# Kernel optimization log

Measured on AMD Instinct MI355X. Metric: run time of the kernel, lower is better.

Reference implementation:

```python
import jax, jax.numpy as jnp
import numpy as np

N = 100000      # nodes
E = 1600000     # edges (avg degree 16)
D_IN = 256
H = 128         # hidden_dim
D_OUT = 64
BN_EPS = 1e-5


def setup_inputs() -> dict:
    key = jax.random.key(0)
    ks = jax.random.split(key, 16)
    s = 0.05  # small init scale
    x = jax.random.normal(ks[0], (N, D_IN), jnp.float32)
    edge_index = jax.random.randint(ks[1], (2, E), 0, N)
    inp = {
        "x": x,
        "edge_index": edge_index,
        "w_in": jax.random.normal(ks[2], (D_IN, H), jnp.float32) * s,
        "b_in": jnp.zeros((H,), jnp.float32),
        # SAGEConv layer 1: lin_l (neighbors, with bias) + lin_r (self, no bias)
        "w_l1": jax.random.normal(ks[3], (H, H), jnp.float32) * s,
        "b_l1": jnp.zeros((H,), jnp.float32),
        "w_r1": jax.random.normal(ks[4], (H, H), jnp.float32) * s,
        "g1": jnp.ones((H,), jnp.float32),
        "be1": jnp.zeros((H,), jnp.float32),
        # SAGEConv layer 2
        "w_l2": jax.random.normal(ks[5], (H, H), jnp.float32) * s,
        "b_l2": jnp.zeros((H,), jnp.float32),
        "w_r2": jax.random.normal(ks[6], (H, H), jnp.float32) * s,
        "g2": jnp.ones((H,), jnp.float32),
        "be2": jnp.zeros((H,), jnp.float32),
        "w_out": jax.random.normal(ks[7], (H, D_OUT), jnp.float32) * s,
        "b_out": jnp.zeros((D_OUT,), jnp.float32),
    }
    return inp


def _sage_conv(x, src, dst, w_l, b_l, w_r):
    # gather messages from source nodes, mean-aggregate at target nodes
    msgs = x[src]                                           # [E, H]
    agg = jax.ops.segment_sum(msgs, dst, num_segments=N)    # [N, H]
    deg = jax.ops.segment_sum(jnp.ones((src.shape[0], 1), x.dtype), dst,
                              num_segments=N)               # [N, 1]
    mean = agg / jnp.maximum(deg, 1.0)
    return mean @ w_l + b_l + x @ w_r


def _bn_eval(h, gamma, beta):
    # BatchNorm1d in eval mode: running_mean=0, running_var=1
    return h * (gamma / jnp.sqrt(1.0 + BN_EPS)) + beta


def reference(x, edge_index, w_in, b_in,
              w_l1, b_l1, w_r1, g1, be1,
              w_l2, b_l2, w_r2, g2, be2,
              w_out, b_out):
    src, dst = edge_index[0], edge_index[1]
    h = jax.nn.relu(x @ w_in + b_in)                         # [N, H]
    h = _sage_conv(h, src, dst, w_l1, b_l1, w_r1)
    h = jax.nn.relu(_bn_eval(h, g1, be1))                    # dropout off (eval)
    h = _sage_conv(h, src, dst, w_l2, b_l2, w_r2)
    h = jax.nn.relu(_bn_eval(h, g2, be2))
    return h @ w_out + b_out                                 # [N, D_OUT]
```

## Files before the change

### kernel.cpp

```cpp
#include <hip/hip_runtime.h>

#define DIN 256
#define H   128
#define DOUT 64

#define EPI_RELU 0
#define EPI_BN   1
#define EPI_NONE 2

#define BKT_SHIFT 7
#define BKT_NODES 128
#define BKT_CAP   4096
#define CSR_CAP   4608

typedef __attribute__((ext_vector_type(8))) short bf16x8;
typedef __attribute__((ext_vector_type(4))) float f32x4;

__device__ inline unsigned short f2bf(float f) {
  union { float f; unsigned u; } v; v.f = f;
  unsigned u = v.u;
  u += 0x7FFFu + ((u >> 16) & 1u);
  return (unsigned short)(u >> 16);
}
__device__ inline float bf2f(unsigned u16) {
  union { unsigned u; float f; } v; v.u = u16 << 16;
  return v.f;
}
__device__ inline unsigned pk_bf16(float lo, float hi) {
  return (unsigned)f2bf(lo) | ((unsigned)f2bf(hi) << 16);
}

#define FILL_TPB 1024
#define FILL_EPT 16
#define FILL_EPB (FILL_TPB * FILL_EPT)

__global__ __launch_bounds__(FILL_TPB) void bucket_fill(
    const int* __restrict__ src, const int* __restrict__ dst,
    int* __restrict__ bcur, unsigned* __restrict__ bedges,
    int nbkt, int e) {
  __shared__ int hist[1024];
  int tid = threadIdx.x;
  int base = blockIdx.x * FILL_EPB;
  for (int i = tid; i < nbkt; i += FILL_TPB) hist[i] = 0;
  __syncthreads();

  int es[FILL_EPT], ed[FILL_EPT];
#pragma unroll
  for (int j = 0; j < FILL_EPT; ++j) {
    int i = base + j * FILL_TPB + tid;
    if (i < e) {
      es[j] = src[i];
      ed[j] = dst[i];
      atomicAdd(&hist[ed[j] >> BKT_SHIFT], 1);
    } else {
      es[j] = -1; ed[j] = 0;
    }
  }
  __syncthreads();
  for (int b = tid; b < nbkt; b += FILL_TPB) {
    int cnt = hist[b];
    hist[b] = cnt ? atomicAdd(&bcur[b], cnt) : 0;
  }
  __syncthreads();
#pragma unroll
  for (int j = 0; j < FILL_EPT; ++j) {
    if (es[j] >= 0) {
      int b = ed[j] >> BKT_SHIFT;
      int p = atomicAdd(&hist[b], 1);
      if (p < BKT_CAP)
        bedges[(size_t)b * BKT_CAP + p] =
            (unsigned)es[j] | ((unsigned)(ed[j] & (BKT_NODES - 1)) << 17);
    }
  }
}

__global__ __launch_bounds__(256) void bucket_sort(
    const int* __restrict__ bcur, const unsigned* __restrict__ bedges,
    int* __restrict__ csr, int2* __restrict__ rowdeg, int n) {
  __shared__ unsigned rec[BKT_CAP];
  __shared__ int srcs[CSR_CAP];
  __shared__ int hist[BKT_NODES];
  __shared__ int cursor[BKT_NODES];
  __shared__ int s_total;
  int tid = threadIdx.x;
  int b = blockIdx.x;
  int cnt = bcur[b];
  if (cnt > BKT_CAP) cnt = BKT_CAP;
  const unsigned* eb = bedges + (size_t)b * BKT_CAP;

  if (tid < BKT_NODES) hist[tid] = 0;
  __syncthreads();
  for (int i = tid; i < cnt; i += 256) {
    unsigned r = eb[i];
    rec[i] = r;
    atomicAdd(&hist[(r >> 17) & 127], 1);
  }
  __syncthreads();
  int myc = (tid < BKT_NODES) ? hist[tid] : 0;
  int myc4 = (myc + 3) & ~3;
  if (tid < BKT_NODES) hist[tid] = myc4;
  __syncthreads();
#pragma unroll
  for (int off = 1; off < BKT_NODES; off <<= 1) {
    int v = 0;
    if (tid < BKT_NODES && tid >= off) v = hist[tid - off];
    __syncthreads();
    if (tid < BKT_NODES) hist[tid] += v;
    __syncthreads();
  }
  int start = 0;
  if (tid < BKT_NODES) {
    start = hist[tid] - myc4;
    cursor[tid] = start;
    int node = b * BKT_NODES + tid;
    if (node < n) rowdeg[node] = make_int2(b * CSR_CAP + start, myc);
    if (tid == BKT_NODES - 1) s_total = hist[tid];
  }
  __syncthreads();
  for (int i = tid; i < cnt; i += 256) {
    unsigned r = rec[i];
    int p = atomicAdd(&cursor[(r >> 17) & 127], 1);
    srcs[p] = (int)(r & 0x1FFFFu);
  }
  if (tid < BKT_NODES) {
    for (int g = start + myc; g < start + myc4; ++g) srcs[g] = 0;
  }
  __syncthreads();
  int total = s_total;
  if (tid < 16 && total + tid < CSR_CAP) srcs[total + tid] = 0;
  __syncthreads();
  int tot16 = total + 16;
  if (tot16 > CSR_CAP) tot16 = CSR_CAP;
  for (int i = tid; i < tot16; i += 256)
    csr[(size_t)b * CSR_CAP + i] = srcs[i];
}

__global__ __launch_bounds__(256) void agg_kernel(
    const unsigned* __restrict__ h, const int2* __restrict__ rowdeg,
    const int* __restrict__ csr, unsigned* __restrict__ mean, int n) {
  int wid = (blockIdx.x * 256 + threadIdx.x) >> 6;
  int lane = threadIdx.x & 63;
  int grp = lane >> 4;
  int c = lane & 15;
  int node = wid * 4 + grp;
  bool valid = node < n;
  if (!valid) node = 0;
  int2 rd = rowdeg[node];
  int beg = rd.x, d = rd.y;

  const uint4* hv = (const uint4*)h;
  float a[8];
#pragma unroll
  for (int k = 0; k < 8; ++k) a[k] = 0.f;

  for (int j0 = 0; j0 < d; j0 += 16) {
    int rem = d - j0;
    const int4* sp = (const int4*)(csr + beg + j0);
    int sv[16];
    *(int4*)&sv[0]  = sp[0];
    *(int4*)&sv[4]  = sp[1];
    *(int4*)&sv[8]  = sp[2];
    *(int4*)&sv[12] = sp[3];
#pragma unroll
    for (int jj = 0; jj < 16; ++jj) {
      float w = (jj < rem) ? 1.f : 0.f;
      uint4 v = hv[(unsigned)(sv[jj] * 16 + c)];
#pragma unroll
      for (int k = 0; k < 4; ++k) {
        unsigned u = ((const unsigned*)&v)[k];
        union { unsigned u; float f; } lo, hi;
        lo.u = u << 16;
        hi.u = u & 0xffff0000u;
        a[2 * k]     = fmaf(w, lo.f, a[2 * k]);
        a[2 * k + 1] = fmaf(w, hi.f, a[2 * k + 1]);
      }
    }
  }

  if (valid) {
    float invd = 1.f / (float)(d > 0 ? d : 1);
    uint4 o;
    o.x = pk_bf16(a[0] * invd, a[1] * invd);
    o.y = pk_bf16(a[2] * invd, a[3] * invd);
    o.z = pk_bf16(a[4] * invd, a[5] * invd);
    o.w = pk_bf16(a[6] * invd, a[7] * invd);
    ((uint4*)mean)[(unsigned)(node * 16 + c)] = o;
  }
}

__global__ __launch_bounds__(256) void prep_w(
    const float* __restrict__ w_in, const float* __restrict__ w_l1,
    const float* __restrict__ w_r1, const float* __restrict__ w_l2,
    const float* __restrict__ w_r2, const float* __restrict__ w_out,
    unsigned short* __restrict__ t_in, unsigned short* __restrict__ t_l1,
    unsigned short* __restrict__ t_r1, unsigned short* __restrict__ t_l2,
    unsigned short* __restrict__ t_r2, unsigned short* __restrict__ t_out) {
  int i = blockIdx.x * 256 + threadIdx.x;
  const float* s; unsigned short* d; int K, M, off;
  if (i < 32768)       { s = w_in;  d = t_in;  K = 256; M = 128; off = i; }
  else if (i < 49152)  { s = w_l1;  d = t_l1;  K = 128; M = 128; off = i - 32768; }
  else if (i < 65536)  { s = w_r1;  d = t_r1;  K = 128; M = 128; off = i - 49152; }
  else if (i < 81920)  { s = w_l2;  d = t_l2;  K = 128; M = 128; off = i - 65536; }
  else if (i < 98304)  { s = w_r2;  d = t_r2;  K = 128; M = 128; off = i - 81920; }
  else if (i < 106496) { s = w_out; d = t_out; K = 128; M = 64;  off = i - 98304; }
  else return;
  int m = off / K, k = off % K;
  d[off] = f2bf(s[(size_t)k * M + m]);
}

template <int K, int M, int NS, int EPI, bool AFP32, bool OUTF32, int MINW>
__global__ __launch_bounds__(256, MINW) void gemm_wave(
    const void* __restrict__ A1, const void* __restrict__ A2,
    const unsigned short* __restrict__ W1, const unsigned short* __restrict__ W2,
    const float* __restrict__ bias, const float* __restrict__ gamma,
    const float* __restrict__ beta, void* __restrict__ Cv,
    int n, int ntiles, int nwaves) {
  constexpr int CG = M / 32;
  constexpr int NT = 2;
  constexpr int KT = K / 32;

  int tid = threadIdx.x, lane = tid & 63, wave = tid >> 6;
  int m16 = lane & 15, quad = lane >> 4;
  int wid = blockIdx.x * 4 + wave;
  int cg = wid & (CG - 1);
  int t0 = wid / CG;
  int tstep = nwaves / CG;

  bf16x8 bf[NS][KT][NT];
#pragma unroll
  for (int s = 0; s < NS; ++s) {
    const unsigned short* Ws = s ? W2 : W1;
#pragma unroll
    for (int kt = 0; kt < KT; ++kt)
#pragma unroll
      for (int tt = 0; tt < NT; ++tt) {
        int col = cg * 32 + tt * 16 + m16;
        bf[s][kt][tt] =
            *(const bf16x8*)(Ws + (size_t)col * K + (kt * 4 + quad) * 8);
      }
  }

  const float inv_std = rsqrtf(1.f + 1e-5f);
  float bv[NT], s2[NT], b2[NT];
#pragma unroll
  for (int tt = 0; tt < NT; ++tt) {
    int col = cg * 32 + tt * 16 + m16;
    bv[tt] = bias[col];
    if constexpr (EPI == EPI_BN) {
      s2[tt] = gamma[col] * inv_std;
      b2[tt] = beta[col];
    } else {
      s2[tt] = 1.f; b2[tt] = 0.f;
    }
  }

  for (int t = t0; t < ntiles; t += tstep) {
    int ra = t * 16 + m16;
    if (ra >= n) ra = n - 1;
    f32x4 acc[NT];
#pragma unroll
    for (int tt = 0; tt < NT; ++tt) acc[tt] = (f32x4){0.f, 0.f, 0.f, 0.f};

    if constexpr (!AFP32) {
      bf16x8 af[NS][KT];
#pragma unroll
      for (int s = 0; s < NS; ++s) {
        const unsigned short* Ap =
            (const unsigned short*)(s ? A2 : A1) + (size_t)ra * K;
#pragma unroll
        for (int kt = 0; kt < KT; ++kt)
          af[s][kt] = *(const bf16x8*)(Ap + (kt * 4 + quad) * 8);
      }
#pragma unroll
      for (int kt = 0; kt < KT; ++kt)
#pragma unroll
        for (int s = 0; s < NS; ++s)
#pragma unroll
          for (int tt = 0; tt < NT; ++tt)
            acc[tt] = __builtin_amdgcn_mfma_f32_16x16x32_bf16(
                af[s][kt], bf[s][kt][tt], acc[tt], 0, 0, 0);
    } else {
      float4 af[KT][2];
      const float* Ap = (const float*)A1 + (size_t)ra * K;
#pragma unroll
      for (int kt = 0; kt < KT; ++kt) {
        af[kt][0] = *(const float4*)(Ap + (kt * 4 + quad) * 8);
        af[kt][1] = *(const float4*)(Ap + (kt * 4 + quad) * 8 + 4);
      }
#pragma unroll
      for (int kt = 0; kt < KT; ++kt) {
        union { unsigned u[4]; bf16x8 v; } pk;
        pk.u[0] = pk_bf16(af[kt][0].x, af[kt][0].y);
        pk.u[1] = pk_bf16(af[kt][0].z, af[kt][0].w);
        pk.u[2] = pk_bf16(af[kt][1].x, af[kt][1].y);
        pk.u[3] = pk_bf16(af[kt][1].z, af[kt][1].w);
#pragma unroll
        for (int tt = 0; tt < NT; ++tt)
          acc[tt] = __builtin_amdgcn_mfma_f32_16x16x32_bf16(
              pk.v, bf[0][kt][tt], acc[tt], 0, 0, 0);
      }
    }

#pragma unroll
    for (int tt = 0; tt < NT; ++tt) {
      int col = cg * 32 + tt * 16 + m16;
#pragma unroll
      for (int r = 0; r < 4; ++r) {
        int row = t * 16 + quad * 4 + r;
        if (row < n) {
          float v = acc[tt][r] + bv[tt];
          if constexpr (EPI == EPI_BN) v = fmaxf(v * s2[tt] + b2[tt], 0.f);
          else if constexpr (EPI == EPI_RELU) v = fmaxf(v, 0.f);
          if constexpr (OUTF32)
            ((float*)Cv)[(size_t)row * M + col] = v;
          else
            ((unsigned short*)Cv)[(size_t)row * M + col] = f2bf(v);
        }
      }
    }
  }
}

extern "C" void kernel_launch(void* const* d_in, const int* in_sizes, int n_in,
                              void* d_out, int out_size, void* d_ws, size_t ws_size,
                              hipStream_t stream) {
  const float* x     = (const float*)d_in[0];
  const int*   ei    = (const int*)d_in[1];
  const float* w_in  = (const float*)d_in[2];
  const float* b_in  = (const float*)d_in[3];
  const float* w_l1  = (const float*)d_in[4];
  const float* b_l1  = (const float*)d_in[5];
  const float* w_r1  = (const float*)d_in[6];
  const float* g1    = (const float*)d_in[7];
  const float* be1   = (const float*)d_in[8];
  const float* w_l2  = (const float*)d_in[9];
  const float* b_l2  = (const float*)d_in[10];
  const float* w_r2  = (const float*)d_in[11];
  const float* g2    = (const float*)d_in[12];
  const float* be2   = (const float*)d_in[13];
  const float* w_out = (const float*)d_in[14];
  const float* b_out = (const float*)d_in[15];
  float* out = (float*)d_out;

  int N = in_sizes[0] / DIN;
  int E = in_sizes[1] / 2;
  const int* src = ei;
  const int* dst = ei + E;
  int nbkt = (N + BKT_NODES - 1) / BKT_NODES;

  char* ws = (char*)d_ws;
  size_t off = 0;
  auto alloc = [&](size_t bytes) -> char* {
    char* p = ws + off;
    off += (bytes + 255) & ~(size_t)255;
    return p;
  };
  unsigned short* buf0 = (unsigned short*)alloc((size_t)N * H * 2);
  unsigned short* buf1 = (unsigned short*)alloc((size_t)N * H * 2);
  unsigned short* buf2 = (unsigned short*)alloc((size_t)N * H * 2);
  int* bcur        = (int*)alloc((size_t)nbkt * 4);
  unsigned* bedges = (unsigned*)alloc((size_t)nbkt * BKT_CAP * 4);
  int* csr         = (int*)alloc((size_t)nbkt * CSR_CAP * 4);
  int2* rowdeg     = (int2*)alloc((size_t)N * 8);
  unsigned short* t_in  = (unsigned short*)alloc(32768 * 2);
  unsigned short* t_l1  = (unsigned short*)alloc(16384 * 2);
  unsigned short* t_r1  = (unsigned short*)alloc(16384 * 2);
  unsigned short* t_l2  = (unsigned short*)alloc(16384 * 2);
  unsigned short* t_r2  = (unsigned short*)alloc(16384 * 2);
  unsigned short* t_out = (unsigned short*)alloc(8192 * 2);
  (void)ws_size;

  hipMemsetAsync(bcur, 0, (size_t)nbkt * 4, stream);
  bucket_fill<<<(E + FILL_EPB - 1) / FILL_EPB, FILL_TPB, 0, stream>>>(
      src, dst, bcur, bedges, nbkt, E);
  bucket_sort<<<nbkt, 256, 0, stream>>>(bcur, bedges, csr, rowdeg, N);
  prep_w<<<(106496 + 255) / 256, 256, 0, stream>>>(
      w_in, w_l1, w_r1, w_l2, w_r2, w_out, t_in, t_l1, t_r1, t_l2, t_r2, t_out);

  int ntiles = (N + 15) / 16;
  int ablocks = (N + 15) / 16;

  gemm_wave<256, 128, 1, EPI_RELU, true, false, 2><<<1024, 256, 0, stream>>>(
      x, nullptr, t_in, nullptr, b_in, nullptr, nullptr, buf0, N, ntiles, 4096);
  agg_kernel<<<ablocks, 256, 0, stream>>>((const unsigned*)buf0, rowdeg,
                                          csr, (unsigned*)buf1, N);
  gemm_wave<128, 128, 2, EPI_BN, false, false, 3><<<768, 256, 0, stream>>>(
      buf1, buf0, t_l1, t_r1, b_l1, g1, be1, buf2, N, ntiles, 3072);
  agg_kernel<<<ablocks, 256, 0, stream>>>((const unsigned*)buf2, rowdeg,
                                          csr, (unsigned*)buf0, N);
  gemm_wave<128, 128, 2, EPI_BN, false, false, 3><<<768, 256, 0, stream>>>(
      buf0, buf2, t_l2, t_r2, b_l2, g2, be2, buf1, N, ntiles, 3072);
  gemm_wave<128, 64, 1, EPI_NONE, false, true, 3><<<768, 256, 0, stream>>>(
      buf1, nullptr, t_out, nullptr, b_out, nullptr, nullptr, out, N, ntiles, 3072);
}
```

Baseline: 456.4 us.

## Stage GEMM weights in LDS with swizzle so each wave computes all output columns

The GEMM kernel previously held a 32-column slice of the bf16 weights in registers per wave, so four waves each reloaded the same A rows. Now each 512-thread block copies the full weight matrix (or both stacked matrices) into LDS with direct global-to-LDS loads, using a rotated-chunk swizzle to avoid bank conflicts. Each wave then computes all M columns of a 16-row tile, so A is read once per tile, and the B fragments are read from LDS per MFMA. The cost is up to 64KB of LDS per block, which limits how many blocks fit per CU, plus extra LDS read traffic in the inner loop.

```diff
diff --git a/kernel.cpp b/kernel.cpp
--- a/kernel.cpp
+++ b/kernel.cpp
@@ -28,6 +28,12 @@
 }
 __device__ inline unsigned pk_bf16(float lo, float hi) {
   return (unsigned)f2bf(lo) | ((unsigned)f2bf(hi) << 16);
+}
+
+__device__ inline void gload_lds16(const void* g, void* l) {
+  __builtin_amdgcn_global_load_lds(
+      (const __attribute__((address_space(1))) void*)g,
+      (__attribute__((address_space(3))) void*)l, 16, 0, 0);
 }
 
 #define FILL_TPB 1024
@@ -208,53 +214,41 @@
   d[off] = f2bf(s[(size_t)k * M + m]);
 }
 
-template <int K, int M, int NS, int EPI, bool AFP32, bool OUTF32, int MINW>
-__global__ __launch_bounds__(256, MINW) void gemm_wave(
+template <int K, int M, int NS, int EPI, bool AFP32, bool OUTF32>
+__global__ __launch_bounds__(512, 4) void gemm_tlp(
     const void* __restrict__ A1, const void* __restrict__ A2,
     const unsigned short* __restrict__ W1, const unsigned short* __restrict__ W2,
     const float* __restrict__ bias, const float* __restrict__ gamma,
     const float* __restrict__ beta, void* __restrict__ Cv,
     int n, int ntiles, int nwaves) {
-  constexpr int CG = M / 32;
-  constexpr int NT = 2;
+  constexpr int NT = M / 16;
   constexpr int KT = K / 32;
+  constexpr int CH = K / 8;
+  constexpr int RPI = 64 / CH;
+  constexpr int NI = (NS * M) / RPI;
+  constexpr int WAVES = 8;
+  __shared__ __align__(16) unsigned short Bs[NS * M * K];
 
   int tid = threadIdx.x, lane = tid & 63, wave = tid >> 6;
   int m16 = lane & 15, quad = lane >> 4;
-  int wid = blockIdx.x * 4 + wave;
-  int cg = wid & (CG - 1);
-  int t0 = wid / CG;
-  int tstep = nwaves / CG;
-
-  bf16x8 bf[NS][KT][NT];
-#pragma unroll
-  for (int s = 0; s < NS; ++s) {
-    const unsigned short* Ws = s ? W2 : W1;
-#pragma unroll
-    for (int kt = 0; kt < KT; ++kt)
-#pragma unroll
-      for (int tt = 0; tt < NT; ++tt) {
-        int col = cg * 32 + tt * 16 + m16;
-        bf[s][kt][tt] =
-            *(const bf16x8*)(Ws + (size_t)col * K + (kt * 4 + quad) * 8);
-      }
-  }
+
+#pragma unroll
+  for (int g = 0; g < NI / WAVES; ++g) {
+    int i = g * WAVES + wave;
+    int r0 = i * RPI;
+    int lr = r0 + lane / CH;
+    int sc = lane & (CH - 1);
+    int cs = (sc - lr) & (CH - 1);
+    const unsigned short* Ws = (NS == 2 && lr >= M) ? W2 : W1;
+    int lrs = lr & (M - 1);
+    gload_lds16(Ws + (size_t)lrs * K + cs * 8, &Bs[r0 * K]);
+  }
+  __syncthreads();
 
   const float inv_std = rsqrtf(1.f + 1e-5f);
-  float bv[NT], s2[NT], b2[NT];
-#pragma unroll
-  for (int tt = 0; tt < NT; ++tt) {
-    int col = cg * 32 + tt * 16 + m16;
-    bv[tt] = bias[col];
-    if constexpr (EPI == EPI_BN) {
-      s2[tt] = gamma[col] * inv_std;
-      b2[tt] = beta[col];
-    } else {
-      s2[tt] = 1.f; b2[tt] = 0.f;
-    }
-  }
-
-  for (int t = t0; t < ntiles; t += tstep) {
+  int wid = blockIdx.x * WAVES + wave;
+
+  for (int t = wid; t < ntiles; t += nwaves) {
     int ra = t * 16 + m16;
     if (ra >= n) ra = n - 1;
     f32x4 acc[NT];
@@ -276,9 +270,13 @@
 #pragma unroll
         for (int s = 0; s < NS; ++s)
 #pragma unroll
-          for (int tt = 0; tt < NT; ++tt)
+          for (int tt = 0; tt < NT; ++tt) {
+            int brow = s * M + tt * 16 + m16;
+            bf16x8 b = *(const bf16x8*)
+                &Bs[brow * K + (((kt * 4 + quad) + brow) & (CH - 1)) * 8];
             acc[tt] = __builtin_amdgcn_mfma_f32_16x16x32_bf16(
-                af[s][kt], bf[s][kt][tt], acc[tt], 0, 0, 0);
+                af[s][kt], b, acc[tt], 0, 0, 0);
+          }
     } else {
       float4 af[KT][2];
       const float* Ap = (const float*)A1 + (size_t)ra * K;
@@ -295,21 +293,31 @@
         pk.u[2] = pk_bf16(af[kt][1].x, af[kt][1].y);
         pk.u[3] = pk_bf16(af[kt][1].z, af[kt][1].w);
 #pragma unroll
-        for (int tt = 0; tt < NT; ++tt)
+        for (int tt = 0; tt < NT; ++tt) {
+          int brow = tt * 16 + m16;
+          bf16x8 b = *(const bf16x8*)
+              &Bs[brow * K + (((kt * 4 + quad) + brow) & (CH - 1)) * 8];
           acc[tt] = __builtin_amdgcn_mfma_f32_16x16x32_bf16(
-              pk.v, bf[0][kt][tt], acc[tt], 0, 0, 0);
+              pk.v, b, acc[tt], 0, 0, 0);
+        }
       }
     }
 
 #pragma unroll
     for (int tt = 0; tt < NT; ++tt) {
-      int col = cg * 32 + tt * 16 + m16;
+      int col = tt * 16 + m16;
+      float bv = bias[col];
+      float s2 = 1.f, b2 = 0.f;
+      if constexpr (EPI == EPI_BN) {
+        s2 = gamma[col] * inv_std;
+        b2 = beta[col];
+      }
 #pragma unroll
       for (int r = 0; r < 4; ++r) {
         int row = t * 16 + quad * 4 + r;
         if (row < n) {
-          float v = acc[tt][r] + bv[tt];
-          if constexpr (EPI == EPI_BN) v = fmaxf(v * s2[tt] + b2[tt], 0.f);
+          float v = acc[tt][r] + bv;
+          if constexpr (EPI == EPI_BN) v = fmaxf(v * s2 + b2, 0.f);
           else if constexpr (EPI == EPI_RELU) v = fmaxf(v, 0.f);
           if constexpr (OUTF32)
             ((float*)Cv)[(size_t)row * M + col] = v;
@@ -379,17 +387,19 @@
 
   int ntiles = (N + 15) / 16;
   int ablocks = (N + 15) / 16;
-
-  gemm_wave<256, 128, 1, EPI_RELU, true, false, 2><<<1024, 256, 0, stream>>>(
-      x, nullptr, t_in, nullptr, b_in, nullptr, nullptr, buf0, N, ntiles, 4096);
+  const int GB = 512;
+  const int NW = GB * 8;
+
+  gemm_tlp<256, 128, 1, EPI_RELU, true, false><<<GB, 512, 0, stream>>>(
+      x, nullptr, t_in, nullptr, b_in, nullptr, nullptr, buf0, N, ntiles, NW);
   agg_kernel<<<ablocks, 256, 0, stream>>>((const unsigned*)buf0, rowdeg,
                                           csr, (unsigned*)buf1, N);
-  gemm_wave<128, 128, 2, EPI_BN, false, false, 3><<<768, 256, 0, stream>>>(
-      buf1, buf0, t_l1, t_r1, b_l1, g1, be1, buf2, N, ntiles, 3072);
+  gemm_tlp<128, 128, 2, EPI_BN, false, false><<<GB, 512, 0, stream>>>(
+      buf1, buf0, t_l1, t_r1, b_l1, g1, be1, buf2, N, ntiles, NW);
   agg_kernel<<<ablocks, 256, 0, stream>>>((const unsigned*)buf2, rowdeg,
                                           csr, (unsigned*)buf0, N);
-  gemm_wave<128, 128, 2, EPI_BN, false, false, 3><<<768, 256, 0, stream>>>(
-      buf0, buf2, t_l2, t_r2, b_l2, g2, be2, buf1, N, ntiles, 3072);
-  gemm_wave<128, 64, 1, EPI_NONE, false, true, 3><<<768, 256, 0, stream>>>(
-      buf1, nullptr, t_out, nullptr, b_out, nullptr, nullptr, out, N, ntiles, 3072);
-}
+  gemm_tlp<128, 128, 2, EPI_BN, false, false><<<GB, 512, 0, stream>>>(
+      buf0, buf2, t_l2, t_r2, b_l2, g2, be2, buf1, N, ntiles, NW);
+  gemm_tlp<128, 64, 1, EPI_NONE, false, true><<<GB, 512, 0, stream>>>(
+      buf1, nullptr, t_out, nullptr, b_out, nullptr, nullptr, out, N, ntiles, NW);
+}
```

Result: slower. 760.0 us (+66.5%).
